# Optimization experiments

Measured on AMD Instinct MI355X. Metric: run time of the kernel, lower is better.

## Reference

```python
import jax, jax.numpy as jnp
import numpy as np

B, NQ, NKV, DQ, DIN = 8, 2048, 2048, 512, 512


def setup_inputs() -> dict:
    key = jax.random.key(0)
    ks = jax.random.split(key, 5)
    scale = 1.0 / np.sqrt(DQ)
    return {
        "query": jax.random.normal(ks[0], (B, NQ, DQ), dtype=jnp.float32),
        "key": jax.random.normal(ks[1], (NKV, DQ), dtype=jnp.float32),
        "x": jax.random.normal(ks[2], (B, NKV, DIN), dtype=jnp.float32),
        "W_proj": jax.random.normal(ks[3], (DQ, DQ), dtype=jnp.float32) * scale,
        "b_proj": jnp.zeros((DQ,), dtype=jnp.float32),
        "W_px": jax.random.normal(ks[4], (DQ, DIN), dtype=jnp.float32) * scale,
        "b_px": jnp.zeros((DQ,), dtype=jnp.float32),
    }


def reference(query, key, x, W_proj, b_proj, W_px, b_px):
    # query_proj = Linear(dim_query, dim_query)(query)            [B, Nq, DQ]
    query_proj = jnp.einsum("bqd,ed->bqe", query, W_proj) + b_proj
    # k = project_x(x) + key.unsqueeze(0)                          [B, Nkv, DQ]
    k = jnp.einsum("bki,ei->bke", x, W_px) + b_px + key[None, :, :]
    # score = bmm(query_proj, k^T)                                 [B, Nq, Nkv]
    score = jnp.einsum("bqe,bke->bqk", query_proj, k)
    # softmax=True branch (note: original applies NO 1/sqrt(d) scaling)
    attn = jax.nn.softmax(score, axis=-1)
    # out = bmm(attn, x)                                           [B, Nq, DIN]
    out = jnp.einsum("bqk,bki->bqi", attn, x)
    return out, attn
```

## Files before the change

### kernel.cpp

```cpp
#include <hip/hip_runtime.h>
#include <hip/hip_bf16.h>

#define B_   8
#define NQ_  2048
#define NKV_ 2048
#define DQ_  512
#define DIN_ 512

using f32x4 = __attribute__((ext_vector_type(4))) float;
using f16   = _Float16;
using f16x4 = __attribute__((ext_vector_type(4))) _Float16;
using f16x8 = __attribute__((ext_vector_type(8))) _Float16;

__device__ __forceinline__ f32x4 mfma16f(f16x8 a, f16x8 b, f32x4 c) {
  return __builtin_amdgcn_mfma_f32_16x16x32_f16(a, b, c, 0, 0, 0);
}

__device__ __forceinline__ void gload_lds16(const void* g, void* l) {
  __builtin_amdgcn_global_load_lds(
      (const __attribute__((address_space(1))) void*)g,
      (__attribute__((address_space(3))) void*)l, 16, 0, 0);
}

__device__ __forceinline__ int xcd_swz(int bid, int nwg) {
  const int c = nwg >> 3;
  return (bid & 7) * c + (bid >> 3);
}

template<int EPI>
__global__ __launch_bounds__(256, 2)
void proj_gemm(const float* __restrict__ A, const float* __restrict__ Bm,
               f16* __restrict__ C,
               const float* __restrict__ bias, const float* __restrict__ keyp)
{
  constexpr int PAD = 8;
  __shared__ f16 Ah[128][64 + PAD];
  __shared__ f16 Bh[128][64 + PAD];

  const int tid  = threadIdx.x;
  const int lane = tid & 63;
  const int w    = tid >> 6;
  const int wr   = w >> 1;
  const int wc   = w & 1;
  const int brow = blockIdx.y * 128;
  const int bcol = blockIdx.x * 128;

  const float* Ag = A  + (size_t)brow * DQ_;
  const float* Bg = Bm + (size_t)bcol * DQ_;

  f32x4 acc[4][4] = {};

  const int sr = tid >> 4;
  const int sc = (tid & 15) * 4;

  float4 pa[8], pb[8];
#pragma unroll
  for (int p = 0; p < 8; ++p) {
    pa[p] = *(const float4*)(Ag + (size_t)(p * 16 + sr) * DQ_ + sc);
    pb[p] = *(const float4*)(Bg + (size_t)(p * 16 + sr) * DQ_ + sc);
  }

  for (int k0 = 0; k0 < DQ_; k0 += 64) {
    __syncthreads();
#pragma unroll
    for (int p = 0; p < 8; ++p) {
      const int r = p * 16 + sr;
      f16x4 ha, hb;
      ha[0] = (f16)pa[p].x; ha[1] = (f16)pa[p].y;
      ha[2] = (f16)pa[p].z; ha[3] = (f16)pa[p].w;
      hb[0] = (f16)pb[p].x; hb[1] = (f16)pb[p].y;
      hb[2] = (f16)pb[p].z; hb[3] = (f16)pb[p].w;
      *(f16x4*)&Ah[r][sc] = ha;
      *(f16x4*)&Bh[r][sc] = hb;
    }
    if (k0 + 64 < DQ_) {
#pragma unroll
      for (int p = 0; p < 8; ++p) {
        pa[p] = *(const float4*)(Ag + (size_t)(p * 16 + sr) * DQ_ + k0 + 64 + sc);
        pb[p] = *(const float4*)(Bg + (size_t)(p * 16 + sr) * DQ_ + k0 + 64 + sc);
      }
    }
    __syncthreads();
#pragma unroll
    for (int kk = 0; kk < 2; ++kk) {
      const int fr = lane & 15;
      const int fc = kk * 32 + (lane >> 4) * 8;
      f16x8 ah[4], bh[4];
#pragma unroll
      for (int m = 0; m < 4; ++m)
        ah[m] = *(const f16x8*)&Ah[wr * 64 + m * 16 + fr][fc];
#pragma unroll
      for (int n = 0; n < 4; ++n)
        bh[n] = *(const f16x8*)&Bh[wc * 64 + n * 16 + fr][fc];
#pragma unroll
      for (int m = 0; m < 4; ++m)
#pragma unroll
        for (int n = 0; n < 4; ++n)
          acc[m][n] = mfma16f(ah[m], bh[n], acc[m][n]);
    }
  }

#pragma unroll
  for (int m = 0; m < 4; ++m)
#pragma unroll
    for (int n = 0; n < 4; ++n)
#pragma unroll
      for (int r = 0; r < 4; ++r) {
        const int row_g = brow + wr * 64 + m * 16 + (lane >> 4) * 4 + r;
        const int col_g = bcol + wc * 64 + n * 16 + (lane & 15);
        float vv = acc[m][n][r] + bias[col_g];
        if (EPI == 2) vv += keyp[(size_t)(row_g & (NKV_ - 1)) * DQ_ + col_g];
        C[(size_t)row_g * DQ_ + col_g] = (f16)vv;
      }
}

__global__ __launch_bounds__(512, 2)
void score_gemm(const f16* __restrict__ qp, const f16* __restrict__ km,
                float* __restrict__ attn)
{
  __shared__ f16 ABuf[2 * 8192];
  __shared__ f16 BBuf[2 * 8192];

  const int swz  = xcd_swz(blockIdx.x, gridDim.x);
  const int bx   = swz & 7;
  const int by   = (swz >> 3) & 7;
  const int b    = swz >> 6;

  const int t    = threadIdx.x;
  const int lane = t & 63;
  const int w    = t >> 6;
  const int wr   = w >> 2;
  const int wcn  = w & 3;
  const int brow = by * 256;
  const int bcol = bx * 256;
  const int fr   = lane & 15;
  const int q    = lane >> 4;
  const int slotE = ((q ^ (fr & 3)) * 8);

  const int srow = t >> 2;
  const int sig  = (t & 3) ^ (srow & 3);
  const f16* aG = qp + ((size_t)b * NQ_  + brow + srow) * DQ_ + sig * 8;
  const f16* bG = km + ((size_t)b * NKV_ + bcol + srow) * DQ_ + sig * 8;

#define STAGE_A(kc) do { \
    const f16* s_ = aG + (kc) * 32; \
    f16* d_ = ABuf + ((kc) & 1) * 8192 + w * 512; \
    gload_lds16(s_, d_); \
    gload_lds16(s_ + (size_t)128 * DQ_, d_ + 4096); } while (0)
#define STAGE_B(kc) do { \
    const f16* s_ = bG + (kc) * 32; \
    f16* d_ = BBuf + ((kc) & 1) * 8192 + w * 512; \
    gload_lds16(s_, d_); \
    gload_lds16(s_ + (size_t)128 * DQ_, d_ + 4096); } while (0)

  f32x4 acc[8][4] = {};

  STAGE_A(0); STAGE_B(0);
  asm volatile("s_waitcnt vmcnt(0)\n\ts_barrier" ::: "memory");

  for (int c = 0; c < 16; ++c) {
    if (c + 1 < 16) { STAGE_A(c + 1); STAGE_B(c + 1); }

    const f16* Ab = ABuf + (c & 1) * 8192;
    const f16* Bb = BBuf + (c & 1) * 8192;

    f16x8 bh[4];
#pragma unroll
    for (int ni = 0; ni < 4; ++ni)
      bh[ni] = *(const f16x8*)&Bb[(wcn * 64 + ni * 16 + fr) * 32 + slotE];

    __builtin_amdgcn_s_setprio(1);
#pragma unroll
    for (int mi = 0; mi < 8; ++mi) {
      const f16x8 ah = *(const f16x8*)&Ab[(wr * 128 + mi * 16 + fr) * 32 + slotE];
#pragma unroll
      for (int ni = 0; ni < 4; ++ni)
        acc[mi][ni] = mfma16f(ah, bh[ni], acc[mi][ni]);
    }
    __builtin_amdgcn_s_setprio(0);

    if (c + 1 < 16)
      asm volatile("s_waitcnt vmcnt(0)\n\ts_barrier" ::: "memory");
  }
#undef STAGE_A
#undef STAGE_B

  float* Cg = attn + (size_t)b * NQ_ * NKV_;
#pragma unroll
  for (int mi = 0; mi < 8; ++mi)
#pragma unroll
    for (int ni = 0; ni < 4; ++ni)
#pragma unroll
      for (int r = 0; r < 4; ++r) {
        const int row_g = brow + wr * 128 + mi * 16 + q * 4 + r;
        const int col_g = bcol + wcn * 64 + ni * 16 + fr;
        Cg[(size_t)row_g * NKV_ + col_g] = acc[mi][ni][r];
      }
}

__global__ __launch_bounds__(256, 2)
void pv_gemm(const f16* __restrict__ attnb, const f16* __restrict__ xT,
             float* __restrict__ out)
{
  __shared__ f16 At[2][128 * 64];
  __shared__ f16 Bt[2][128 * 64];

  const int swz  = xcd_swz(blockIdx.x, gridDim.x);
  const int bx   = swz & 3;
  const int by   = (swz >> 2) & 15;
  const int b    = swz >> 6;

  const int t    = threadIdx.x;
  const int lane = t & 63;
  const int w    = t >> 6;
  const int wr   = w >> 1;
  const int wc   = w & 1;
  const int brow = by * 128;
  const int bcol = bx * 128;

  const int srow  = t >> 3;
  const int sslot = t & 7;
  const int sig   = sslot ^ (srow & 7);
  const f16* aG = attnb + ((size_t)b * NQ_ + brow + srow) * NKV_ + sig * 8;
  const f16* bG = xT + (size_t)b * DIN_ * NKV_ + (size_t)(bcol + srow) * NKV_ + sig * 8;

  f32x4 acc[4][4] = {};
  const int fr = lane & 15;
  const int q  = lane >> 4;

#define PV_STAGE(ks, buf) do { \
    const f16* a_ = aG + (size_t)(ks) * 64; \
    const f16* b_ = bG + (size_t)(ks) * 64; \
    f16* al_ = At[buf] + w * 512; \
    f16* bl_ = Bt[buf] + w * 512; \
    _Pragma("unroll") for (int i = 0; i < 4; ++i) { \
      gload_lds16(a_ + (size_t)i * 32 * NKV_, al_ + i * 2048); \
      gload_lds16(b_ + (size_t)i * 32 * NKV_, bl_ + i * 2048); } } while (0)

  PV_STAGE(0, 0);
  asm volatile("s_waitcnt vmcnt(0)\n\ts_barrier" ::: "memory");

  for (int ks = 0; ks < NKV_ / 64; ++ks) {
    const int cur = ks & 1;
    if (ks + 1 < NKV_ / 64) PV_STAGE(ks + 1, cur ^ 1);

    const f16* Ac = At[cur];
    const f16* Bc = Bt[cur];
#pragma unroll
    for (int kk = 0; kk < 2; ++kk) {
      f16x8 ah[4], bh[4];
#pragma unroll
      for (int m = 0; m < 4; ++m) {
        const int rt = wr * 64 + m * 16 + fr;
        ah[m] = *(const f16x8*)&Ac[rt * 64 + (((kk * 4 + q) ^ (rt & 7)) * 8)];
      }
#pragma unroll
      for (int n = 0; n < 4; ++n) {
        const int rt = wc * 64 + n * 16 + fr;
        bh[n] = *(const f16x8*)&Bc[rt * 64 + (((kk * 4 + q) ^ (rt & 7)) * 8)];
      }
#pragma unroll
      for (int m = 0; m < 4; ++m)
#pragma unroll
        for (int n = 0; n < 4; ++n)
          acc[m][n] = mfma16f(ah[m], bh[n], acc[m][n]);
    }
    asm volatile("s_waitcnt vmcnt(0)\n\ts_barrier" ::: "memory");
  }
#undef PV_STAGE

  float* Cg = out + (size_t)b * NQ_ * DIN_;
#pragma unroll
  for (int m = 0; m < 4; ++m)
#pragma unroll
    for (int n = 0; n < 4; ++n)
#pragma unroll
      for (int r = 0; r < 4; ++r) {
        const int row_g = brow + wr * 64 + m * 16 + q * 4 + r;
        const int col_g = bcol + wc * 64 + n * 16 + fr;
        Cg[(size_t)row_g * DIN_ + col_g] = acc[m][n][r];
      }
}

__global__ void transpose_x(const float* __restrict__ x, f16* __restrict__ xT)
{
  __shared__ float tile[32][33];
  const int b  = blockIdx.z;
  const int j0 = blockIdx.x * 32;
  const int i0 = blockIdx.y * 32;
  const float* xs = x  + (size_t)b * NKV_ * DIN_;
  f16*         xd = xT + (size_t)b * DIN_ * NKV_;
  const int tx = threadIdx.x, ty = threadIdx.y;
#pragma unroll
  for (int p = 0; p < 32; p += 8)
    tile[ty + p][tx] = xs[(size_t)(j0 + ty + p) * DIN_ + i0 + tx];
  __syncthreads();
#pragma unroll
  for (int p = 0; p < 32; p += 8)
    xd[(size_t)(i0 + ty + p) * NKV_ + j0 + tx] = (f16)tile[tx][ty + p];
}

__global__ void softmax_rows(float* __restrict__ attn, f16* __restrict__ attnb)
{
  const int lane = threadIdx.x & 63;
  const int wv   = threadIdx.x >> 6;
  const size_t row = (size_t)blockIdx.x * 4 + wv;
  float* p  = attn  + row * NKV_;
  f16*   pb = attnb + row * NKV_;

  float4 v[8];
  float mx = -1e30f;
#pragma unroll
  for (int i = 0; i < 8; ++i) {
    v[i] = *(const float4*)&p[i * 256 + lane * 4];
    mx = fmaxf(mx, fmaxf(fmaxf(v[i].x, v[i].y), fmaxf(v[i].z, v[i].w)));
  }
#pragma unroll
  for (int off = 32; off; off >>= 1) mx = fmaxf(mx, __shfl_xor(mx, off, 64));

  float sum = 0.f;
#pragma unroll
  for (int i = 0; i < 8; ++i) {
    v[i].x = expf(v[i].x - mx);
    v[i].y = expf(v[i].y - mx);
    v[i].z = expf(v[i].z - mx);
    v[i].w = expf(v[i].w - mx);
    sum += v[i].x + v[i].y + v[i].z + v[i].w;
  }
#pragma unroll
  for (int off = 32; off; off >>= 1) sum += __shfl_xor(sum, off, 64);

  const float inv = 1.0f / sum;
#pragma unroll
  for (int i = 0; i < 8; ++i) {
    v[i].x *= inv; v[i].y *= inv; v[i].z *= inv; v[i].w *= inv;
    *(float4*)&p[i * 256 + lane * 4] = v[i];
    f16x4 hv;
    hv[0] = (f16)v[i].x; hv[1] = (f16)v[i].y;
    hv[2] = (f16)v[i].z; hv[3] = (f16)v[i].w;
    *(f16x4*)&pb[i * 256 + lane * 4] = hv;
  }
}

extern "C" void kernel_launch(void* const* d_in, const int* in_sizes, int n_in,
                              void* d_out, int out_size, void* d_ws, size_t ws_size,
                              hipStream_t stream)
{
  (void)in_sizes; (void)n_in; (void)out_size; (void)ws_size;
  const float* query  = (const float*)d_in[0];
  const float* key    = (const float*)d_in[1];
  const float* x      = (const float*)d_in[2];
  const float* W_proj = (const float*)d_in[3];
  const float* b_proj = (const float*)d_in[4];
  const float* W_px   = (const float*)d_in[5];
  const float* b_px   = (const float*)d_in[6];

  float* out  = (float*)d_out;
  float* attn = out + (size_t)B_ * NQ_ * DIN_;

  const size_t PQE = (size_t)B_ * NQ_ * DQ_;
  f16* xT = (f16*)d_ws;
  f16* qp = xT + PQE;
  f16* km = qp + PQE;
  f16* attnb = qp;

  transpose_x<<<dim3(NKV_ / 32, DIN_ / 32, B_), dim3(32, 8), 0, stream>>>(x, xT);

  proj_gemm<1><<<dim3(DQ_ / 128, (B_ * NQ_) / 128, 1), 256, 0, stream>>>(
      query, W_proj, qp, b_proj, nullptr);

  proj_gemm<2><<<dim3(DQ_ / 128, (B_ * NQ_) / 128, 1), 256, 0, stream>>>(
      x, W_px, km, b_px, key);

  score_gemm<<<(NKV_ / 256) * (NQ_ / 256) * B_, 512, 0, stream>>>(qp, km, attn);

  softmax_rows<<<(B_ * NQ_) / 4, 256, 0, stream>>>(attn, attnb);

  pv_gemm<<<(DIN_ / 128) * (NQ_ / 128) * B_, 256, 0, stream>>>(attnb, xT, out);
}
```

Before: 225.8 us.

## Fuse x transpose into projection GEMM and merge both projections into one launch

Drops the standalone transpose_x kernel. The blocks that project x with blockIdx.x==0 now write the fp16 transposed x tile from the LDS staging buffer at each k-step. The two projection GEMMs become one launch using gridDim.z=2, with runtime selection of pointers and epilogue. This removes one full read of x, one launch, and a serialization point between launches. The cost is extra strided LDS reads and global stores in a subset of blocks, which adds load imbalance, plus runtime branching in place of a template parameter.

```diff
diff --git a/kernel.cpp b/kernel.cpp
--- a/kernel.cpp
+++ b/kernel.cpp
@@ -27,15 +27,22 @@
   return (bid & 7) * c + (bid >> 3);
 }
 
-template<int EPI>
 __global__ __launch_bounds__(256, 2)
-void proj_gemm(const float* __restrict__ A, const float* __restrict__ Bm,
-               f16* __restrict__ C,
-               const float* __restrict__ bias, const float* __restrict__ keyp)
+void proj_gemm(const float* __restrict__ query, const float* __restrict__ W_proj,
+               const float* __restrict__ b_proj, f16* __restrict__ qp,
+               const float* __restrict__ x, const float* __restrict__ W_px,
+               const float* __restrict__ b_px, const float* __restrict__ keyp,
+               f16* __restrict__ km, f16* __restrict__ xTp)
 {
   constexpr int PAD = 8;
   __shared__ f16 Ah[128][64 + PAD];
   __shared__ f16 Bh[128][64 + PAD];
+
+  const bool second = (blockIdx.z == 1);
+  const float* A    = second ? x    : query;
+  const float* Bm   = second ? W_px : W_proj;
+  const float* bias = second ? b_px : b_proj;
+  f16*         C    = second ? km   : qp;
 
   const int tid  = threadIdx.x;
   const int lane = tid & 63;
@@ -59,6 +66,8 @@
     pa[p] = *(const float4*)(Ag + (size_t)(p * 16 + sr) * DQ_ + sc);
     pb[p] = *(const float4*)(Bg + (size_t)(p * 16 + sr) * DQ_ + sc);
   }
+
+  const bool emitXT = second && (blockIdx.x == 0);
 
   for (int k0 = 0; k0 < DQ_; k0 += 64) {
     __syncthreads();
@@ -98,6 +107,20 @@
         for (int n = 0; n < 4; ++n)
           acc[m][n] = mfma16f(ah[m], bh[n], acc[m][n]);
     }
+
+    if (emitXT) {
+      const int dl = tid >> 2;
+      const int j0 = (tid & 3) * 32;
+      f16* dst = xTp + ((size_t)(brow >> 11) * DIN_ + k0 + dl) * NKV_
+                     + (brow & (NKV_ - 1)) + j0;
+#pragma unroll
+      for (int v = 0; v < 4; ++v) {
+        f16x8 tv;
+#pragma unroll
+        for (int e = 0; e < 8; ++e) tv[e] = Ah[j0 + v * 8 + e][dl];
+        *(f16x8*)(dst + v * 8) = tv;
+      }
+    }
   }
 
 #pragma unroll
@@ -109,7 +132,7 @@
         const int row_g = brow + wr * 64 + m * 16 + (lane >> 4) * 4 + r;
         const int col_g = bcol + wc * 64 + n * 16 + (lane & 15);
         float vv = acc[m][n][r] + bias[col_g];
-        if (EPI == 2) vv += keyp[(size_t)(row_g & (NKV_ - 1)) * DQ_ + col_g];
+        if (second) vv += keyp[(size_t)(row_g & (NKV_ - 1)) * DQ_ + col_g];
         C[(size_t)row_g * DQ_ + col_g] = (f16)vv;
       }
 }
@@ -282,24 +305,6 @@
       }
 }
 
-__global__ void transpose_x(const float* __restrict__ x, f16* __restrict__ xT)
-{
-  __shared__ float tile[32][33];
-  const int b  = blockIdx.z;
-  const int j0 = blockIdx.x * 32;
-  const int i0 = blockIdx.y * 32;
-  const float* xs = x  + (size_t)b * NKV_ * DIN_;
-  f16*         xd = xT + (size_t)b * DIN_ * NKV_;
-  const int tx = threadIdx.x, ty = threadIdx.y;
-#pragma unroll
-  for (int p = 0; p < 32; p += 8)
-    tile[ty + p][tx] = xs[(size_t)(j0 + ty + p) * DIN_ + i0 + tx];
-  __syncthreads();
-#pragma unroll
-  for (int p = 0; p < 32; p += 8)
-    xd[(size_t)(i0 + ty + p) * NKV_ + j0 + tx] = (f16)tile[tx][ty + p];
-}
-
 __global__ void softmax_rows(float* __restrict__ attn, f16* __restrict__ attnb)
 {
   const int lane = threadIdx.x & 63;
@@ -364,13 +369,8 @@
   f16* km = qp + PQE;
   f16* attnb = qp;
 
-  transpose_x<<<dim3(NKV_ / 32, DIN_ / 32, B_), dim3(32, 8), 0, stream>>>(x, xT);
-
-  proj_gemm<1><<<dim3(DQ_ / 128, (B_ * NQ_) / 128, 1), 256, 0, stream>>>(
-      query, W_proj, qp, b_proj, nullptr);
-
-  proj_gemm<2><<<dim3(DQ_ / 128, (B_ * NQ_) / 128, 1), 256, 0, stream>>>(
-      x, W_px, km, b_px, key);
+  proj_gemm<<<dim3(DQ_ / 128, (B_ * NQ_) / 128, 2), 256, 0, stream>>>(
+      query, W_proj, b_proj, qp, x, W_px, b_px, key, km, xT);
 
   score_gemm<<<(NKV_ / 256) * (NQ_ / 256) * B_, 512, 0, stream>>>(qp, km, attn);
 
```

Measured after the change: 227.4 us. No clear change (+0.7%).
